# Kernel optimization log

Hardware: AMD Instinct MI355X
Metric: run time of the kernel (lower is better)

Reference implementation:

```python
import jax, jax.numpy as jnp
import numpy as np

B, S, E, H = 2, 2048, 1024, 16
D = E // H  # head_dim = 64


def setup_inputs() -> dict:
    key = jax.random.key(0)
    ks = jax.random.split(key, 7)
    scale = 1.0 / np.sqrt(E)
    return {
        "q": jax.random.normal(ks[0], (B, S, E), jnp.float32),
        "k": jax.random.normal(ks[1], (B, S, E), jnp.float32),
        "v": jax.random.normal(ks[2], (B, S, E), jnp.float32),
        "Wq": jax.random.normal(ks[3], (E, E), jnp.float32) * scale,
        "bq": jnp.zeros((E,), jnp.float32),
        "Wk": jax.random.normal(ks[4], (E, E), jnp.float32) * scale,
        "bk": jnp.zeros((E,), jnp.float32),
        "Wv": jax.random.normal(ks[5], (E, E), jnp.float32) * scale,
        "bv": jnp.zeros((E,), jnp.float32),
        "Wo": jax.random.normal(ks[6], (E, E), jnp.float32) * scale,
        "bo": jnp.zeros((E,), jnp.float32),
    }


def _split_heads(x):
    # [B, S, E] -> [B, H, S, D]
    b, s, _ = x.shape
    return x.reshape(b, s, H, D).transpose(0, 2, 1, 3)


def reference(q, k, v, Wq, bq, Wk, bk, Wv, bv, Wo, bo):
    qh = _split_heads(q @ Wq + bq)  # [B,H,S,D]
    kh = _split_heads(k @ Wk + bk)
    vh = _split_heads(v @ Wv + bv)
    scores = jnp.einsum("bhqd,bhkd->bhqk", qh, kh) / jnp.sqrt(jnp.float32(D))
    # causal mask, TF band_part(ones, -1, 0) == lower triangular
    mask = jnp.tril(jnp.ones((S, S), jnp.float32))
    scores = scores * mask - 1e9 * (1.0 - mask)
    weights = jax.nn.softmax(scores, axis=-1)
    attn = jnp.einsum("bhqk,bhkd->bhqd", weights, vh)  # [B,H,S,D]
    concat = attn.transpose(0, 2, 1, 3).reshape(q.shape[0], S, E)
    return concat @ Wo + bo
```

## Files before the change

### kernel.cpp

```cpp
#include <hip/hip_runtime.h>
#include <math.h>

#define Bd 2
#define Sd 2048
#define Ed 1024
#define Hd 16
#define Dd 64
#define Md (Bd * Sd)
#define Kd 1024
#define Nd 1024

typedef __attribute__((ext_vector_type(8))) short bf16x8;
typedef __attribute__((ext_vector_type(4))) float f32x4;

__device__ __forceinline__ unsigned short f2bf(float f) {
    unsigned x = __float_as_uint(f);
    x += 0x7fffu + ((x >> 16) & 1u);
    return (unsigned short)(x >> 16);
}

__device__ __forceinline__ unsigned pk_bf16_rhu(float a, float b) {
    return __builtin_amdgcn_perm(__float_as_uint(b) + 0x8000u,
                                 __float_as_uint(a) + 0x8000u, 0x07060302u);
}

__device__ __forceinline__ void gl2lds16(const unsigned short* g, unsigned short* l) {
    __builtin_amdgcn_global_load_lds(
        (__attribute__((address_space(1))) void*)g,
        (__attribute__((address_space(3))) void*)l, 16, 0, 0);
}

__global__ __launch_bounds__(256) void prep_k(
    const float* __restrict__ q, const float* __restrict__ k, const float* __restrict__ v,
    unsigned short* __restrict__ qb, unsigned short* __restrict__ kb,
    unsigned short* __restrict__ vb,
    const float* __restrict__ w0, const float* __restrict__ w1,
    const float* __restrict__ w2, const float* __restrict__ w3,
    unsigned short* __restrict__ o0, unsigned short* __restrict__ o1,
    unsigned short* __restrict__ o2, unsigned short* __restrict__ o3)
{
    const int bx = blockIdx.x;
    if (bx < 3072) {
        const int zz = bx >> 10;
        const int blk = bx & 1023;
        const float* s = zz == 0 ? q : zz == 1 ? k : v;
        unsigned short* d = zz == 0 ? qb : zz == 1 ? kb : vb;
        const int n4 = (Bd * Sd * Ed) / 4;
        int i = blk * 256 + threadIdx.x;
        for (; i < n4; i += 1024 * 256) {
            float4 x = ((const float4*)s)[i];
            uint2 u = make_uint2(pk_bf16_rhu(x.x, x.y), pk_bf16_rhu(x.z, x.w));
            ((uint2*)d)[i] = u;
        }
        return;
    }
    __shared__ unsigned short Tl[32][36];
    const int idx = bx - 3072;
    const int z   = idx >> 10;
    const int ky  = (idx >> 5) & 31;
    const int nx  = idx & 31;
    const float* W = z == 0 ? w0 : z == 1 ? w1 : z == 2 ? w2 : w3;
    unsigned short* Wt = z == 0 ? o0 : z == 1 ? o1 : z == 2 ? o2 : o3;

    const int t = threadIdx.x;
    const int r = t >> 3;
    const int c4 = (t & 7) * 4;
    const int k0 = ky * 32;
    const int n0 = nx * 32;

    float4 x = *(const float4*)(W + (size_t)(k0 + r) * Nd + n0 + c4);
    Tl[c4 + 0][r] = f2bf(x.x);
    Tl[c4 + 1][r] = f2bf(x.y);
    Tl[c4 + 2][r] = f2bf(x.z);
    Tl[c4 + 3][r] = f2bf(x.w);
    __syncthreads();
    ushort4 u = make_ushort4(Tl[r][c4 + 0], Tl[r][c4 + 1], Tl[r][c4 + 2], Tl[r][c4 + 3]);
    *(ushort4*)(Wt + (size_t)(n0 + r) * Kd + k0 + c4) = u;
}

template <int AM>
__device__ __forceinline__ void gemm_v5(
    const unsigned short* __restrict__ A, const unsigned short* __restrict__ Bt,
    const float* __restrict__ bias, void* __restrict__ Yv,
    int m0, int n0, int mode, float oscale)
{
    constexpr int AMT = AM / 32;
    __shared__ unsigned short As[2][AM * 32];
    __shared__ unsigned short Bs[2][128 * 32];

    const int tid  = threadIdx.x;
    const int w    = tid >> 6;
    const int lane = tid & 63;
    const int ln   = lane & 15;
    const int quad = lane >> 4;
    const int wm = (w >> 1) * (AM / 2);
    const int wn = (w & 1) * 64;

    const int lrow = lane >> 2;
    const int lcol = (lane & 3) * 8;

    const unsigned short* Bg0 = Bt + (size_t)(n0 + (2 * w) * 16 + lrow) * Kd + lcol;
    const unsigned short* Bg1 = Bg0 + 16 * Kd;
    const int aseg = (AM == 128) ? 2 * w : w;
    const unsigned short* Ag0 = A + (size_t)(m0 + aseg * 16 + lrow) * Kd + lcol;
    const unsigned short* Ag1 = Ag0 + 16 * Kd;

    f32x4 acc[AMT][4];
    #pragma unroll
    for (int i = 0; i < AMT; ++i)
        #pragma unroll
        for (int j = 0; j < 4; ++j)
            acc[i][j] = (f32x4){0.f, 0.f, 0.f, 0.f};

    gl2lds16(Bg0, &Bs[0][(2 * w) * 512]);
    gl2lds16(Bg1, &Bs[0][(2 * w) * 512 + 512]);
    gl2lds16(Ag0, &As[0][aseg * 512]);
    if constexpr (AM == 128) gl2lds16(Ag1, &As[0][aseg * 512 + 512]);

    for (int k0 = 0; k0 < Kd; k0 += 32) {
        const int buf = (k0 >> 5) & 1;
        __syncthreads();

        if (k0 + 32 < Kd) {
            gl2lds16(Bg0 + k0 + 32, &Bs[buf ^ 1][(2 * w) * 512]);
            gl2lds16(Bg1 + k0 + 32, &Bs[buf ^ 1][(2 * w) * 512 + 512]);
            gl2lds16(Ag0 + k0 + 32, &As[buf ^ 1][aseg * 512]);
            if constexpr (AM == 128)
                gl2lds16(Ag1 + k0 + 32, &As[buf ^ 1][aseg * 512 + 512]);
        }

        bf16x8 af[AMT], bfr[4];
        #pragma unroll
        for (int mi = 0; mi < AMT; ++mi)
            af[mi] = *(const bf16x8*)(&As[buf][(wm + mi * 16 + ln) * 32 + quad * 8]);
        #pragma unroll
        for (int ni = 0; ni < 4; ++ni)
            bfr[ni] = *(const bf16x8*)(&Bs[buf][(wn + ni * 16 + ln) * 32 + quad * 8]);
        #pragma unroll
        for (int mi = 0; mi < AMT; ++mi)
            #pragma unroll
            for (int ni = 0; ni < 4; ++ni)
                acc[mi][ni] = __builtin_amdgcn_mfma_f32_16x16x32_bf16(
                    af[mi], bfr[ni], acc[mi][ni], 0, 0, 0);
    }

    float bval[4];
    #pragma unroll
    for (int ni = 0; ni < 4; ++ni) bval[ni] = bias[n0 + wn + ni * 16 + ln];

    if (mode == 0) {
        float* Y = (float*)Yv;
        #pragma unroll
        for (int mi = 0; mi < AMT; ++mi) {
            #pragma unroll
            for (int ni = 0; ni < 4; ++ni) {
                int n = n0 + wn + ni * 16 + ln;
                #pragma unroll
                for (int r = 0; r < 4; ++r) {
                    int m = m0 + wm + mi * 16 + quad * 4 + r;
                    Y[(size_t)m * Nd + n] = (acc[mi][ni][r] + bval[ni]) * oscale;
                }
            }
        }
    } else if (mode == 1) {
        unsigned short* Y = (unsigned short*)Yv;
        #pragma unroll
        for (int mi = 0; mi < AMT; ++mi) {
            #pragma unroll
            for (int ni = 0; ni < 4; ++ni) {
                int n = n0 + wn + ni * 16 + ln;
                int h = n >> 6, d = n & 63;
                #pragma unroll
                for (int r = 0; r < 4; ++r) {
                    int m = m0 + wm + mi * 16 + quad * 4 + r;
                    int b = m >> 11, s = m & 2047;
                    Y[(((size_t)b * Hd + h) * Sd + s) * Dd + d] =
                        f2bf((acc[mi][ni][r] + bval[ni]) * oscale);
                }
            }
        }
    } else {
        unsigned short* Y = (unsigned short*)Yv;
        #pragma unroll
        for (int mi = 0; mi < AMT; ++mi) {
            int mbase = m0 + wm + mi * 16 + quad * 4;
            int b = mbase >> 11, s = mbase & 2047;
            #pragma unroll
            for (int ni = 0; ni < 4; ++ni) {
                int n = n0 + wn + ni * 16 + ln;
                int h = n >> 6, d = n & 63;
                ushort4 u = make_ushort4(
                    f2bf((acc[mi][ni][0] + bval[ni]) * oscale),
                    f2bf((acc[mi][ni][1] + bval[ni]) * oscale),
                    f2bf((acc[mi][ni][2] + bval[ni]) * oscale),
                    f2bf((acc[mi][ni][3] + bval[ni]) * oscale));
                *(ushort4*)(Y + (((size_t)b * Hd + h) * Dd + d) * Sd + s) = u;
            }
        }
    }
}

__global__ __launch_bounds__(256) void proj_gemm_k(
    const unsigned short* A0, const unsigned short* A1, const unsigned short* A2,
    const unsigned short* B0, const unsigned short* B1, const unsigned short* B2,
    const float* b0, const float* b1, const float* b2,
    unsigned short* Y0, unsigned short* Y1, unsigned short* Y2)
{
    const int l    = blockIdx.x;
    const int xcd  = l & 7;
    const int g    = l >> 3;
    const int n_t  = g & 7;
    const int msub = (g >> 3) & 3;
    const int z    = g >> 5;
    const int m_t  = xcd * 4 + msub;

    const unsigned short* A = z == 0 ? A0 : z == 1 ? A1 : A2;
    const unsigned short* B = z == 0 ? B0 : z == 1 ? B1 : B2;
    const float* bias       = z == 0 ? b0 : z == 1 ? b1 : b2;
    unsigned short* Y       = z == 0 ? Y0 : z == 1 ? Y1 : Y2;
    gemm_v5<128>(A, B, bias, Y, m_t * 128, n_t * 128,
                 z == 2 ? 2 : 1,
                 z == 0 ? 0.18033688011112042f : 1.0f);
}

__global__ __launch_bounds__(256) void out_gemm_k(
    const unsigned short* A, const unsigned short* Bt, const float* bias, float* Y)
{
    const int l    = blockIdx.x;
    const int xcd  = l & 7;
    const int g    = l >> 3;
    const int n_t  = g & 7;
    const int msub = g >> 3;
    const int m_t  = xcd * 8 + msub;
    gemm_v5<64>(A, Bt, bias, Y, m_t * 64, n_t * 128, 0, 1.0f);
}

__global__ __launch_bounds__(256) void attn_mfma_k(
    const unsigned short* __restrict__ Qg,
    const unsigned short* __restrict__ Kg,
    const unsigned short* __restrict__ Vg,
    unsigned short* __restrict__ Aout)
{
    __shared__ unsigned short Ks[2][64 * 64];
    __shared__ unsigned short Vs[2][64 * 64];
    __shared__ unsigned short Pt[4][16][72];

    const int tid  = threadIdx.x;
    const int w    = tid >> 6;
    const int lane = tid & 63;
    const int ln   = lane & 15;
    const int quad = lane >> 4;

    const int l   = blockIdx.x;
    const int bh  = (l & 7) * 4 + ((l >> 3) & 3);
    const int qtA = l >> 5;
    const int b   = bh >> 4;
    const int h   = bh & 15;

    const size_t baseQK = (size_t)bh * Sd * Dd;
    const size_t baseV  = (size_t)bh * Dd * Sd;
    const f32x4 vzero = {0.f, 0.f, 0.f, 0.f};

    const int qtB = 31 - qtA;
    const int nA  = qtA + 1;

    const int sr = lane >> 3;
    const int sc = ((lane & 7) ^ sr) * 8;
    const int rb0 = w * 16, rb1 = w * 16 + 8;
    const int swl = ln & 7;
    const int c0 = ((quad    ) ^ swl) * 8;
    const int c1 = ((quad + 4) ^ swl) * 8;

    const int qrowA = qtA * 64 + w * 16;
    const int qrowB = qtB * 64 + w * 16;
    const unsigned short* qpA = Qg + baseQK + (size_t)(qrowA + ln) * Dd + 8 * quad;
    const unsigned short* qpB = Qg + baseQK + (size_t)(qrowB + ln) * Dd + 8 * quad;
    const bf16x8 qA0 = *(const bf16x8*)(qpA), qA1 = *(const bf16x8*)(qpA + 32);
    const bf16x8 qB0 = *(const bf16x8*)(qpB), qB1 = *(const bf16x8*)(qpB + 32);

    float l_lane = 0.f;
    f32x4 O[4];
    #pragma unroll
    for (int t = 0; t < 4; ++t) O[t] = vzero;

    gl2lds16(Kg + baseQK + (size_t)(rb0 + sr) * Dd + sc, &Ks[0][rb0 * 64]);
    gl2lds16(Kg + baseQK + (size_t)(rb1 + sr) * Dd + sc, &Ks[0][rb1 * 64]);
    gl2lds16(Vg + baseV  + (size_t)(rb0 + sr) * Sd + sc, &Vs[0][rb0 * 64]);
    gl2lds16(Vg + baseV  + (size_t)(rb1 + sr) * Sd + sc, &Vs[0][rb1 * 64]);

    for (int it = 0; it < 33; ++it) {
        const int cur = it & 1;
        __syncthreads();

        if (it + 1 < 33) {
            const int nk = ((it + 1 < nA) ? (it + 1) : (it + 1 - nA)) * 64;
            gl2lds16(Kg + baseQK + (size_t)(nk + rb0 + sr) * Dd + sc, &Ks[cur ^ 1][rb0 * 64]);
            gl2lds16(Kg + baseQK + (size_t)(nk + rb1 + sr) * Dd + sc, &Ks[cur ^ 1][rb1 * 64]);
            gl2lds16(Vg + baseV  + (size_t)(rb0 + sr) * Sd + nk + sc, &Vs[cur ^ 1][rb0 * 64]);
            gl2lds16(Vg + baseV  + (size_t)(rb1 + sr) * Sd + nk + sc, &Vs[cur ^ 1][rb1 * 64]);
        }

        const bool inA   = (it < nA);
        const int  krow  = (inA ? it : it - nA) * 64;
        const bool diag  = inA ? (it == nA - 1) : (it == 32);
        const int  qglob = (inA ? qrowA : qrowB) + ln;
        const bf16x8 qf0 = inA ? qA0 : qB0;
        const bf16x8 qf1 = inA ? qA1 : qB1;

        f32x4 S[4];
        #pragma unroll
        for (int t = 0; t < 4; ++t) {
            const int R = (t * 16 + ln) * 64;
            bf16x8 k0 = *(const bf16x8*)&Ks[cur][R + c0];
            bf16x8 k1 = *(const bf16x8*)&Ks[cur][R + c1];
            f32x4 z = __builtin_amdgcn_mfma_f32_16x16x32_bf16(k0, qf0, vzero, 0, 0, 0);
            S[t]     = __builtin_amdgcn_mfma_f32_16x16x32_bf16(k1, qf1, z,     0, 0, 0);
        }

        if (diag) {
            #pragma unroll
            for (int t = 0; t < 4; ++t)
                #pragma unroll
                for (int r = 0; r < 4; ++r)
                    if (krow + t * 16 + quad * 4 + r > qglob)
                        S[t][r] = -1e30f;
        }

        float p[16];
        float rsum = 0.f;
        #pragma unroll
        for (int t = 0; t < 4; ++t) {
            #pragma unroll
            for (int r = 0; r < 4; ++r) {
                float e = __builtin_amdgcn_exp2f(S[t][r]);
                p[t * 4 + r] = e;
                rsum += e;
            }
        }
        l_lane += rsum;

        #pragma unroll
        for (int t = 0; t < 4; ++t) {
            uint2 u = make_uint2(pk_bf16_rhu(p[t * 4 + 0], p[t * 4 + 1]),
                                 pk_bf16_rhu(p[t * 4 + 2], p[t * 4 + 3]));
            *(uint2*)&Pt[w][ln][t * 16 + quad * 4] = u;
        }
        bf16x8 pf0 = *(const bf16x8*)&Pt[w][ln][8 * quad];
        bf16x8 pf1 = *(const bf16x8*)&Pt[w][ln][32 + 8 * quad];

        #pragma unroll
        for (int t = 0; t < 4; ++t) {
            const int R = (t * 16 + ln) * 64;
            bf16x8 v0 = *(const bf16x8*)&Vs[cur][R + c0];
            bf16x8 v1 = *(const bf16x8*)&Vs[cur][R + c1];
            O[t] = __builtin_amdgcn_mfma_f32_16x16x32_bf16(v0, pf0, O[t], 0, 0, 0);
            O[t] = __builtin_amdgcn_mfma_f32_16x16x32_bf16(v1, pf1, O[t], 0, 0, 0);
        }

        if (it == nA - 1) {
            float l_run = l_lane;
            l_run += __shfl_xor(l_run, 16);
            l_run += __shfl_xor(l_run, 32);
            float inv = 1.f / l_run;
            unsigned short* op =
                Aout + ((size_t)b * Sd + qrowA + ln) * Ed + h * 64 + quad * 4;
            #pragma unroll
            for (int t = 0; t < 4; ++t) {
                ushort4 u = make_ushort4(f2bf(O[t][0] * inv), f2bf(O[t][1] * inv),
                                         f2bf(O[t][2] * inv), f2bf(O[t][3] * inv));
                *(ushort4*)(op + t * 16) = u;
            }
            l_lane = 0.f;
            #pragma unroll
            for (int t = 0; t < 4; ++t) O[t] = vzero;
        }
    }

    float l_run = l_lane;
    l_run += __shfl_xor(l_run, 16);
    l_run += __shfl_xor(l_run, 32);
    float inv = 1.f / l_run;
    unsigned short* op = Aout + ((size_t)b * Sd + qrowB + ln) * Ed + h * 64 + quad * 4;
    #pragma unroll
    for (int t = 0; t < 4; ++t) {
        ushort4 u = make_ushort4(f2bf(O[t][0] * inv), f2bf(O[t][1] * inv),
                                 f2bf(O[t][2] * inv), f2bf(O[t][3] * inv));
        *(ushort4*)(op + t * 16) = u;
    }
}

extern "C" void kernel_launch(void* const* d_in, const int* in_sizes, int n_in,
                              void* d_out, int out_size, void* d_ws, size_t ws_size,
                              hipStream_t stream) {
    const float* q  = (const float*)d_in[0];
    const float* k  = (const float*)d_in[1];
    const float* v  = (const float*)d_in[2];
    const float* Wq = (const float*)d_in[3];
    const float* bq = (const float*)d_in[4];
    const float* Wk = (const float*)d_in[5];
    const float* bk = (const float*)d_in[6];
    const float* Wv = (const float*)d_in[7];
    const float* bv = (const float*)d_in[8];
    const float* Wo = (const float*)d_in[9];
    const float* bo = (const float*)d_in[10];

    const size_t TENS = (size_t)Bd * Sd * Ed;
    const size_t WE   = (size_t)Ed * Ed;
    unsigned short* qb  = (unsigned short*)d_ws;
    unsigned short* kb  = qb + TENS;
    unsigned short* vb  = kb + TENS;
    unsigned short* Wqt = vb + TENS;
    unsigned short* Wkt = Wqt + WE;
    unsigned short* Wvt = Wkt + WE;
    unsigned short* Wot = Wvt + WE;
    unsigned short* Qh  = Wot + WE;
    unsigned short* Kh  = Qh + TENS;
    unsigned short* Vt  = Kh + TENS;
    unsigned short* An  = Vt + TENS;

    prep_k<<<dim3(7168), 256, 0, stream>>>(q, k, v, qb, kb, vb,
                                           Wq, Wk, Wv, Wo, Wqt, Wkt, Wvt, Wot);
    proj_gemm_k<<<dim3(768), 256, 0, stream>>>(
        qb, kb, vb, Wqt, Wkt, Wvt, bq, bk, bv, Qh, Kh, Vt);
    attn_mfma_k<<<dim3(512), 256, 0, stream>>>(Qh, Kh, Vt, An);
    out_gemm_k<<<dim3(512), 256, 0, stream>>>(An, Wot, bo, (float*)d_out);
}
```

Baseline: 206.7 us.

## Fuse fp32-to-bf16 activation conversion into projection GEMM A-tile loads

After: 241.1 us. +16.6%, slower.

```diff
diff --git a/kernel.cpp b/kernel.cpp
--- a/kernel.cpp
+++ b/kernel.cpp
@@ -30,32 +30,24 @@
         (__attribute__((address_space(3))) void*)l, 16, 0, 0);
 }
 
+__device__ __forceinline__ void packA8(const float4& a, const float4& b,
+                                       unsigned short* dst) {
+    uint4 u;
+    u.x = pk_bf16_rhu(a.x, a.y);
+    u.y = pk_bf16_rhu(a.z, a.w);
+    u.z = pk_bf16_rhu(b.x, b.y);
+    u.w = pk_bf16_rhu(b.z, b.w);
+    *(uint4*)dst = u;
+}
+
 __global__ __launch_bounds__(256) void prep_k(
-    const float* __restrict__ q, const float* __restrict__ k, const float* __restrict__ v,
-    unsigned short* __restrict__ qb, unsigned short* __restrict__ kb,
-    unsigned short* __restrict__ vb,
     const float* __restrict__ w0, const float* __restrict__ w1,
     const float* __restrict__ w2, const float* __restrict__ w3,
     unsigned short* __restrict__ o0, unsigned short* __restrict__ o1,
     unsigned short* __restrict__ o2, unsigned short* __restrict__ o3)
 {
-    const int bx = blockIdx.x;
-    if (bx < 3072) {
-        const int zz = bx >> 10;
-        const int blk = bx & 1023;
-        const float* s = zz == 0 ? q : zz == 1 ? k : v;
-        unsigned short* d = zz == 0 ? qb : zz == 1 ? kb : vb;
-        const int n4 = (Bd * Sd * Ed) / 4;
-        int i = blk * 256 + threadIdx.x;
-        for (; i < n4; i += 1024 * 256) {
-            float4 x = ((const float4*)s)[i];
-            uint2 u = make_uint2(pk_bf16_rhu(x.x, x.y), pk_bf16_rhu(x.z, x.w));
-            ((uint2*)d)[i] = u;
-        }
-        return;
-    }
     __shared__ unsigned short Tl[32][36];
-    const int idx = bx - 3072;
+    const int idx = blockIdx.x;
     const int z   = idx >> 10;
     const int ky  = (idx >> 5) & 31;
     const int nx  = idx & 31;
@@ -78,14 +70,12 @@
     *(ushort4*)(Wt + (size_t)(n0 + r) * Kd + k0 + c4) = u;
 }
 
-template <int AM>
-__device__ __forceinline__ void gemm_v5(
-    const unsigned short* __restrict__ A, const unsigned short* __restrict__ Bt,
-    const float* __restrict__ bias, void* __restrict__ Yv,
+__device__ __forceinline__ void gemm_af32(
+    const float* __restrict__ Ap, const unsigned short* __restrict__ Bt,
+    const float* __restrict__ bias, unsigned short* __restrict__ Y,
     int m0, int n0, int mode, float oscale)
 {
-    constexpr int AMT = AM / 32;
-    __shared__ unsigned short As[2][AM * 32];
+    __shared__ unsigned short As[2][128 * 32];
     __shared__ unsigned short Bs[2][128 * 32];
 
     const int tid  = threadIdx.x;
@@ -93,7 +83,7 @@
     const int lane = tid & 63;
     const int ln   = lane & 15;
     const int quad = lane >> 4;
-    const int wm = (w >> 1) * (AM / 2);
+    const int wm = (w >> 1) * 64;
     const int wn = (w & 1) * 64;
 
     const int lrow = lane >> 2;
@@ -101,71 +91,77 @@
 
     const unsigned short* Bg0 = Bt + (size_t)(n0 + (2 * w) * 16 + lrow) * Kd + lcol;
     const unsigned short* Bg1 = Bg0 + 16 * Kd;
-    const int aseg = (AM == 128) ? 2 * w : w;
-    const unsigned short* Ag0 = A + (size_t)(m0 + aseg * 16 + lrow) * Kd + lcol;
-    const unsigned short* Ag1 = Ag0 + 16 * Kd;
-
-    f32x4 acc[AMT][4];
-    #pragma unroll
-    for (int i = 0; i < AMT; ++i)
+    const float* A32g0 = Ap + (size_t)(m0 + (2 * w) * 16 + lrow) * Kd + lcol;
+    const float* A32g1 = A32g0 + 16 * Kd;
+    const int aoff = (2 * w) * 512 + lrow * 32 + lcol;
+
+    f32x4 acc[4][4];
+    #pragma unroll
+    for (int i = 0; i < 4; ++i)
         #pragma unroll
         for (int j = 0; j < 4; ++j)
             acc[i][j] = (f32x4){0.f, 0.f, 0.f, 0.f};
 
     gl2lds16(Bg0, &Bs[0][(2 * w) * 512]);
     gl2lds16(Bg1, &Bs[0][(2 * w) * 512 + 512]);
-    gl2lds16(Ag0, &As[0][aseg * 512]);
-    if constexpr (AM == 128) gl2lds16(Ag1, &As[0][aseg * 512 + 512]);
-
-    for (int k0 = 0; k0 < Kd; k0 += 32) {
-        const int buf = (k0 >> 5) & 1;
+    {
+        float4 a0 = *(const float4*)(A32g0);
+        float4 a1 = *(const float4*)(A32g0 + 4);
+        float4 b0 = *(const float4*)(A32g1);
+        float4 b1 = *(const float4*)(A32g1 + 4);
+        packA8(a0, a1, &As[0][aoff]);
+        packA8(b0, b1, &As[0][aoff + 512]);
+    }
+    float4 rr[2][4];
+    rr[1][0] = *(const float4*)(A32g0 + 32);
+    rr[1][1] = *(const float4*)(A32g0 + 36);
+    rr[1][2] = *(const float4*)(A32g1 + 32);
+    rr[1][3] = *(const float4*)(A32g1 + 36);
+
+    #pragma unroll 2
+    for (int i = 0; i < 32; ++i) {
+        const int k0  = i * 32;
+        const int buf = i & 1;
         __syncthreads();
 
-        if (k0 + 32 < Kd) {
+        if (i + 1 < 32) {
             gl2lds16(Bg0 + k0 + 32, &Bs[buf ^ 1][(2 * w) * 512]);
             gl2lds16(Bg1 + k0 + 32, &Bs[buf ^ 1][(2 * w) * 512 + 512]);
-            gl2lds16(Ag0 + k0 + 32, &As[buf ^ 1][aseg * 512]);
-            if constexpr (AM == 128)
-                gl2lds16(Ag1 + k0 + 32, &As[buf ^ 1][aseg * 512 + 512]);
-        }
-
-        bf16x8 af[AMT], bfr[4];
-        #pragma unroll
-        for (int mi = 0; mi < AMT; ++mi)
+        }
+        if (i + 2 < 32) {
+            rr[buf][0] = *(const float4*)(A32g0 + k0 + 64);
+            rr[buf][1] = *(const float4*)(A32g0 + k0 + 68);
+            rr[buf][2] = *(const float4*)(A32g1 + k0 + 64);
+            rr[buf][3] = *(const float4*)(A32g1 + k0 + 68);
+        }
+
+        bf16x8 af[4], bfr[4];
+        #pragma unroll
+        for (int mi = 0; mi < 4; ++mi)
             af[mi] = *(const bf16x8*)(&As[buf][(wm + mi * 16 + ln) * 32 + quad * 8]);
         #pragma unroll
         for (int ni = 0; ni < 4; ++ni)
             bfr[ni] = *(const bf16x8*)(&Bs[buf][(wn + ni * 16 + ln) * 32 + quad * 8]);
         #pragma unroll
-        for (int mi = 0; mi < AMT; ++mi)
+        for (int mi = 0; mi < 4; ++mi)
             #pragma unroll
             for (int ni = 0; ni < 4; ++ni)
                 acc[mi][ni] = __builtin_amdgcn_mfma_f32_16x16x32_bf16(
                     af[mi], bfr[ni], acc[mi][ni], 0, 0, 0);
+
+        if (i + 1 < 32) {
+            packA8(rr[buf ^ 1][0], rr[buf ^ 1][1], &As[buf ^ 1][aoff]);
+            packA8(rr[buf ^ 1][2], rr[buf ^ 1][3], &As[buf ^ 1][aoff + 512]);
+        }
     }
 
     float bval[4];
     #pragma unroll
     for (int ni = 0; ni < 4; ++ni) bval[ni] = bias[n0 + wn + ni * 16 + ln];
 
-    if (mode == 0) {
-        float* Y = (float*)Yv;
-        #pragma unroll
-        for (int mi = 0; mi < AMT; ++mi) {
-            #pragma unroll
-            for (int ni = 0; ni < 4; ++ni) {
-                int n = n0 + wn + ni * 16 + ln;
-                #pragma unroll
-                for (int r = 0; r < 4; ++r) {
-                    int m = m0 + wm + mi * 16 + quad * 4 + r;
-                    Y[(size_t)m * Nd + n] = (acc[mi][ni][r] + bval[ni]) * oscale;
-                }
-            }
-        }
-    } else if (mode == 1) {
-        unsigned short* Y = (unsigned short*)Yv;
-        #pragma unroll
-        for (int mi = 0; mi < AMT; ++mi) {
+    if (mode == 1) {
+        #pragma unroll
+        for (int mi = 0; mi < 4; ++mi) {
             #pragma unroll
             for (int ni = 0; ni < 4; ++ni) {
                 int n = n0 + wn + ni * 16 + ln;
@@ -180,9 +176,8 @@
             }
         }
     } else {
-        unsigned short* Y = (unsigned short*)Yv;
-        #pragma unroll
-        for (int mi = 0; mi < AMT; ++mi) {
+        #pragma unroll
+        for (int mi = 0; mi < 4; ++mi) {
             int mbase = m0 + wm + mi * 16 + quad * 4;
             int b = mbase >> 11, s = mbase & 2047;
             #pragma unroll
@@ -200,8 +195,93 @@
     }
 }
 
+template <int AM>
+__device__ __forceinline__ void gemm_v5(
+    const unsigned short* __restrict__ A, const unsigned short* __restrict__ Bt,
+    const float* __restrict__ bias, void* __restrict__ Yv,
+    int m0, int n0, float oscale)
+{
+    constexpr int AMT = AM / 32;
+    __shared__ unsigned short As[2][AM * 32];
+    __shared__ unsigned short Bs[2][128 * 32];
+
+    const int tid  = threadIdx.x;
+    const int w    = tid >> 6;
+    const int lane = tid & 63;
+    const int ln   = lane & 15;
+    const int quad = lane >> 4;
+    const int wm = (w >> 1) * (AM / 2);
+    const int wn = (w & 1) * 64;
+
+    const int lrow = lane >> 2;
+    const int lcol = (lane & 3) * 8;
+
+    const unsigned short* Bg0 = Bt + (size_t)(n0 + (2 * w) * 16 + lrow) * Kd + lcol;
+    const unsigned short* Bg1 = Bg0 + 16 * Kd;
+    const int aseg = (AM == 128) ? 2 * w : w;
+    const unsigned short* Ag0 = A + (size_t)(m0 + aseg * 16 + lrow) * Kd + lcol;
+    const unsigned short* Ag1 = Ag0 + 16 * Kd;
+
+    f32x4 acc[AMT][4];
+    #pragma unroll
+    for (int i = 0; i < AMT; ++i)
+        #pragma unroll
+        for (int j = 0; j < 4; ++j)
+            acc[i][j] = (f32x4){0.f, 0.f, 0.f, 0.f};
+
+    gl2lds16(Bg0, &Bs[0][(2 * w) * 512]);
+    gl2lds16(Bg1, &Bs[0][(2 * w) * 512 + 512]);
+    gl2lds16(Ag0, &As[0][aseg * 512]);
+    if constexpr (AM == 128) gl2lds16(Ag1, &As[0][aseg * 512 + 512]);
+
+    for (int k0 = 0; k0 < Kd; k0 += 32) {
+        const int buf = (k0 >> 5) & 1;
+        __syncthreads();
+
+        if (k0 + 32 < Kd) {
+            gl2lds16(Bg0 + k0 + 32, &Bs[buf ^ 1][(2 * w) * 512]);
+            gl2lds16(Bg1 + k0 + 32, &Bs[buf ^ 1][(2 * w) * 512 + 512]);
+            gl2lds16(Ag0 + k0 + 32, &As[buf ^ 1][aseg * 512]);
+            if constexpr (AM == 128)
+                gl2lds16(Ag1 + k0 + 32, &As[buf ^ 1][aseg * 512 + 512]);
+        }
+
+        bf16x8 af[AMT], bfr[4];
+        #pragma unroll
+        for (int mi = 0; mi < AMT; ++mi)
+            af[mi] = *(const bf16x8*)(&As[buf][(wm + mi * 16 + ln) * 32 + quad * 8]);
+        #pragma unroll
+        for (int ni = 0; ni < 4; ++ni)
+            bfr[ni] = *(const bf16x8*)(&Bs[buf][(wn + ni * 16 + ln) * 32 + quad * 8]);
+        #pragma unroll
+        for (int mi = 0; mi < AMT; ++mi)
+            #pragma unroll
+            for (int ni = 0; ni < 4; ++ni)
+                acc[mi][ni] = __builtin_amdgcn_mfma_f32_16x16x32_bf16(
+                    af[mi], bfr[ni], acc[mi][ni], 0, 0, 0);
+    }
+
+    float bval[4];
+    #pragma unroll
+    for (int ni = 0; ni < 4; ++ni) bval[ni] = bias[n0 + wn + ni * 16 + ln];
+
+    float* Y = (float*)Yv;
+    #pragma unroll
+    for (int mi = 0; mi < AMT; ++mi) {
+        #pragma unroll
+        for (int ni = 0; ni < 4; ++ni) {
+            int n = n0 + wn + ni * 16 + ln;
+            #pragma unroll
+            for (int r = 0; r < 4; ++r) {
+                int m = m0 + wm + mi * 16 + quad * 4 + r;
+                Y[(size_t)m * Nd + n] = (acc[mi][ni][r] + bval[ni]) * oscale;
+            }
+        }
+    }
+}
+
 __global__ __launch_bounds__(256) void proj_gemm_k(
-    const unsigned short* A0, const unsigned short* A1, const unsigned short* A2,
+    const float* A0, const float* A1, const float* A2,
     const unsigned short* B0, const unsigned short* B1, const unsigned short* B2,
     const float* b0, const float* b1, const float* b2,
     unsigned short* Y0, unsigned short* Y1, unsigned short* Y2)
@@ -214,13 +294,13 @@
     const int z    = g >> 5;
     const int m_t  = xcd * 4 + msub;
 
-    const unsigned short* A = z == 0 ? A0 : z == 1 ? A1 : A2;
+    const float* A          = z == 0 ? A0 : z == 1 ? A1 : A2;
     const unsigned short* B = z == 0 ? B0 : z == 1 ? B1 : B2;
     const float* bias       = z == 0 ? b0 : z == 1 ? b1 : b2;
     unsigned short* Y       = z == 0 ? Y0 : z == 1 ? Y1 : Y2;
-    gemm_v5<128>(A, B, bias, Y, m_t * 128, n_t * 128,
-                 z == 2 ? 2 : 1,
-                 z == 0 ? 0.18033688011112042f : 1.0f);
+    gemm_af32(A, B, bias, Y, m_t * 128, n_t * 128,
+              z == 2 ? 2 : 1,
+              z == 0 ? 0.18033688011112042f : 1.0f);
 }
 
 __global__ __launch_bounds__(256) void out_gemm_k(
@@ -232,7 +312,7 @@
     const int n_t  = g & 7;
     const int msub = g >> 3;
     const int m_t  = xcd * 8 + msub;
-    gemm_v5<64>(A, Bt, bias, Y, m_t * 64, n_t * 128, 0, 1.0f);
+    gemm_v5<64>(A, Bt, bias, Y, m_t * 64, n_t * 128, 1.0f);
 }
 
 __global__ __launch_bounds__(256) void attn_mfma_k(
@@ -406,10 +486,7 @@
 
     const size_t TENS = (size_t)Bd * Sd * Ed;
     const size_t WE   = (size_t)Ed * Ed;
-    unsigned short* qb  = (unsigned short*)d_ws;
-    unsigned short* kb  = qb + TENS;
-    unsigned short* vb  = kb + TENS;
-    unsigned short* Wqt = vb + TENS;
+    unsigned short* Wqt = (unsigned short*)d_ws;
     unsigned short* Wkt = Wqt + WE;
     unsigned short* Wvt = Wkt + WE;
     unsigned short* Wot = Wvt + WE;
@@ -418,10 +495,9 @@
     unsigned short* Vt  = Kh + TENS;
     unsigned short* An  = Vt + TENS;
 
-    prep_k<<<dim3(7168), 256, 0, stream>>>(q, k, v, qb, kb, vb,
-                                           Wq, Wk, Wv, Wo, Wqt, Wkt, Wvt, Wot);
+    prep_k<<<dim3(4096), 256, 0, stream>>>(Wq, Wk, Wv, Wo, Wqt, Wkt, Wvt, Wot);
     proj_gemm_k<<<dim3(768), 256, 0, stream>>>(
-        qb, kb, vb, Wqt, Wkt, Wvt, bq, bk, bv, Qh, Kh, Vt);
+        q, k, v, Wqt, Wkt, Wvt, bq, bk, bv, Qh, Kh, Vt);
     attn_mfma_k<<<dim3(512), 256, 0, stream>>>(Qh, Kh, Vt, An);
     out_gemm_k<<<dim3(512), 256, 0, stream>>>(An, Wot, bo, (float*)d_out);
 }
```
